# Kernel tuning notes

Hardware: AMD Instinct MI355X
Metric: run time of the kernel (lower is better)

Reference implementation:

```python
import jax, jax.numpy as jnp
import numpy as np

EPS = 1e-5
NEG = -1e9

def _ln(x, g, b):
    m = x.mean(-1, keepdims=True)
    v = ((x - m) ** 2).mean(-1, keepdims=True)
    return (x - m) / jnp.sqrt(v + EPS) * g + b

def setup_inputs() -> dict:
    key = jax.random.key(0)
    ks = jax.random.split(key, 32)
    B, N, D, F, L = 2, 512, 128, 512, 3
    s = 0.05
    rn = lambda k, sh, sc=s: jax.random.normal(k, sh, jnp.float32) * sc
    inp = {
        'rel_matrix': rn(ks[0], (B, N, N, 2), 1.0),
        'pre_w': rn(ks[1], (2, D)), 'pre_b': rn(ks[2], (D,)),
        'proj_w': rn(ks[3], (2 * D, D)), 'proj_b': rn(ks[4], (D,)),
        'out_w1': rn(ks[5], (D, D)),
        'bn_g': 1.0 + rn(ks[6], (D,)), 'bn_b': rn(ks[7], (D,)),
        'bn_m': rn(ks[8], (D,)),
        'bn_v': 0.5 + jax.random.uniform(ks[9], (D,), jnp.float32),
        'out_w2': rn(ks[10], (D, D)), 'out_b2': rn(ks[11], (D,)),
        'pe': rn(ks[12], (128, D)),
        'wq': rn(ks[13], (L, D, D)), 'bq': rn(ks[14], (L, D)),
        'wk': rn(ks[15], (L, D, D)), 'bk': rn(ks[16], (L, D)),
        'wv': rn(ks[17], (L, D, D)), 'bv': rn(ks[18], (L, D)),
        'wo': rn(ks[19], (L, D, D)), 'bo': rn(ks[20], (L, D)),
        'ln1g': jnp.ones((L, D), jnp.float32), 'ln1b': jnp.zeros((L, D), jnp.float32),
        'ln2g': jnp.ones((L, D), jnp.float32), 'ln2b': jnp.zeros((L, D), jnp.float32),
        'fw1': rn(ks[21], (L, D, F)), 'fb1': rn(ks[22], (L, F)),
        'fw2': rn(ks[23], (L, F, D)), 'fb2': rn(ks[24], (L, D)),
        'mask': jax.random.randint(ks[25], (B, N), 0, 2) > 0,
        'agent_id': jax.random.randint(ks[26], (B, N), 0, 128, dtype=jnp.int32),
    }
    return inp

def reference(rel_matrix, pre_w, pre_b, proj_w, proj_b, out_w1, bn_g, bn_b, bn_m, bn_v,
              out_w2, out_b2, pe, wq, bq, wk, bk, wv, bv, wo, bo,
              ln1g, ln1b, ln2g, ln2b, fw1, fb1, fw2, fb2, mask, agent_id):
    # --- pairwise relation chain (the headroom target) ---
    # symmetric pairwise validity mask (B,N,N)
    pm = (mask[:, None, :] & mask[:, :, None]).astype(rel_matrix.dtype)
    count = jnp.maximum(pm.sum(axis=2), 1.0)  # (B,N) valid-partner counts
    x = rel_matrix @ pre_w + pre_b            # (B,N,N,D) pre_proj Linear(2->128)
    pooled = jnp.einsum('bijd,bij->bid', x, pm) / count[..., None]  # masked mean over j
    x = jnp.concatenate([x, jnp.broadcast_to(pooled[:, :, None, :], x.shape)], axis=-1)
    x = x @ proj_w + proj_b                   # Linear(256->128)
    x = jnp.einsum('bijd,bij->bid', x, pm) / count[..., None]       # masked mean over j
    # out MLP: Linear(no bias) + BatchNorm1d(eval) + ReLU + Linear
    h = x @ out_w1
    h = (h - bn_m) / jnp.sqrt(bn_v + EPS) * bn_g + bn_b
    x = jax.nn.relu(h) @ out_w2 + out_b2
    x = x + pe[agent_id]                      # agent positional embedding
    # --- 3 post-norm single-head transformer layers (eval, dropout off) ---
    kbias = jnp.where(mask, 0.0, NEG)[:, None, :]  # key padding bias (B,1,N)
    scale = 1.0 / jnp.sqrt(jnp.asarray(x.shape[-1], x.dtype))
    for l in range(3):
        q = x @ wq[l] + bq[l]
        k = x @ wk[l] + bk[l]
        v = x @ wv[l] + bv[l]
        a = jax.nn.softmax(jnp.einsum('bid,bjd->bij', q, k) * scale + kbias, axis=-1)
        att = jnp.einsum('bij,bjd->bid', a, v) @ wo[l] + bo[l]
        x = _ln(x + att, ln1g[l], ln1b[l])
        ff = jax.nn.relu(x @ fw1[l] + fb1[l]) @ fw2[l] + fb2[l]
        x = _ln(x + ff, ln2g[l], ln2b[l])
    return x
```

## Files before the change

### kernel.cpp

```cpp
#include <hip/hip_runtime.h>
#include <hip/hip_bf16.h>

typedef unsigned short u16;
typedef unsigned int u32;
typedef unsigned char u8;
typedef __attribute__((ext_vector_type(8))) short bf16x8;
typedef __attribute__((ext_vector_type(4))) float f32x4;

#define DEV __device__ __forceinline__

DEV float bf2f(u16 u) { union { u32 i; float f; } c; c.i = ((u32)u) << 16; return c.f; }
DEV u16 f2bf(float f) {
  union { float f; u32 i; } c; c.f = f;
  u32 r = c.i + 0x7FFFu + ((c.i >> 16) & 1u);
  return (u16)(r >> 16);
}
DEV u32 pk2(float lo, float hi) { return (u32)f2bf(lo) | ((u32)f2bf(hi) << 16); }
DEV float rdsrc(const void* p, int e, int isb) {
  return isb ? bf2f(((const u16*)p)[e]) : ((const float*)p)[e];
}
DEV bf16x8 as_bf(uint4 v) { union { uint4 u; bf16x8 h; } c; c.u = v; return c.h; }

static constexpr int B = 2, N = 512, D = 128, F = 512;
static constexpr int NROW = B * N;
static constexpr float EPS = 1e-5f;
static constexpr float NEG = -1e9f;
static constexpr float SCALE = 0.08838834764831845f;

#define OFF_PRE_W   0
#define OFF_PRE_B   256
#define OFF_PROJ_B  33152
#define OFF_BN_G    49664
#define OFF_BN_B    49792
#define OFF_BN_M    49920
#define OFF_BN_V    50048
#define OFF_OUT_B2  66560
#define OFF_PE      66688
#define OFF_BQ      132224
#define OFF_BK      181760
#define OFF_BV      231296
#define OFF_BO      280832
#define OFF_LN1G    281216
#define OFF_LN1B    281600
#define OFF_LN2G    281984
#define OFF_LN2B    282368
#define OFF_FB1     479360
#define OFF_FB2     677504
#define W_TOTAL     677888

static constexpr int PB_PROJ = 0;
static constexpr int PB_OW1  = 8192;
static constexpr int PB_OW2  = 16384;
static constexpr int PB_L0   = 24576;
static constexpr int PB_LSTR = 98304;
static constexpr int PB_WO   = 24576;
static constexpr int PB_FW1  = 32768;
static constexpr int PB_FW2  = 65536;
static constexpr int PTOT    = 79872;

struct NEnt { const void* s; int off, n; };
struct PEnt { const void* s1; const void* s2; int o1, o2, dst, lgn, cum; };
struct PrepArgs { NEnt nrm[19]; PEnt pk[21]; };

template<int KT>
DEV f32x4 mmaK(const uint4* __restrict__ aPk, const uint4* __restrict__ Bp,
               int ncol, int col, int lane) {
  f32x4 acc = {0.f, 0.f, 0.f, 0.f};
  const int sub = lane >> 4;
  #pragma unroll
  for (int kt = 0; kt < KT; ++kt) {
    const int e8 = kt * 4 + sub;
    acc = __builtin_amdgcn_mfma_f32_16x16x32_bf16(
        as_bf(aPk[e8 * 16 + (lane & 15)]),
        as_bf(Bp[(size_t)e8 * ncol + col]),
        acc, 0, 0, 0);
  }
  return acc;
}

DEV void packA(const float* __restrict__ src, int ld, int K,
               uint4* __restrict__ aPk, int t) {
  const int n = (K >> 3) * 4;
  for (int i = t; i < n; i += 512) {
    const int e8 = i >> 2, r = i & 3;
    const float* s = src + r * ld + e8 * 8;
    uint4 w;
    w.x = pk2(s[0], s[1]); w.y = pk2(s[2], s[3]);
    w.z = pk2(s[4], s[5]); w.w = pk2(s[6], s[7]);
    aPk[e8 * 16 + r] = w;
  }
}

__global__ __launch_bounds__(256) void k_prep(PrepArgs pa,
    const void* __restrict__ bnv, const void* __restrict__ maskp,
    int* __restrict__ flags, int* __restrict__ mbuf,
    float* __restrict__ W, u32* __restrict__ Wb)
{
  const int t = threadIdx.x, bid = blockIdx.x;
  __shared__ int s_nb, s_m4, s_m2;
  if (t == 0) { s_nb = 0; s_m4 = 0; s_m2 = 0; }
  __syncthreads();
  if (t < 64) {
    const u32 w = ((const u32*)bnv)[t];
    if (((w >> 8) & 0xFFu) != 0x3Fu || ((w >> 24) & 0xFFu) != 0x3Fu)
      atomicOr(&s_nb, 1);
  }
  __syncthreads();
  const int isb = s_nb ? 0 : 1;

  if (bid < 16) {
    for (int ten = 0; ten < 19; ++ten) {
      const NEnt E = pa.nrm[ten];
      for (int e = bid * 256 + t; e < E.n; e += 16 * 256)
        W[E.off + e] = rdsrc(E.s, e, isb);
    }
  } else if (bid < 143) {
    for (int g = (bid - 16) * 256 + t; g < PTOT; g += 127 * 256) {
      int ei = 0;
      #pragma unroll
      for (int k = 1; k < 21; ++k) if (g >= pa.pk[k].cum) ei = k;
      const PEnt E = pa.pk[ei];
      const int li = g - E.cum;
      const int e8 = li >> E.lgn, c = li & ((1 << E.lgn) - 1);
      float f[8];
      #pragma unroll
      for (int i = 0; i < 8; ++i) {
        const int si = ((e8 * 8 + i) << E.lgn) + c;
        f[i] = rdsrc(E.s1, E.o1 + si, isb);
        if (E.s2) f[i] += rdsrc(E.s2, E.o2 + si, isb);
      }
      uint4 w;
      w.x = pk2(f[0], f[1]); w.y = pk2(f[2], f[3]);
      w.z = pk2(f[4], f[5]); w.w = pk2(f[6], f[7]);
      ((uint4*)(Wb + E.dst))[li] = w;
    }
  } else {
    {
      const u32 w = ((const u32*)maskp)[t];
      if (!(w == 0u || w == 1u || w == 0x3F800000u)) atomicOr(&s_m4, 1);
      if (!(w == 0u || w == 1u || w == 0x10000u || w == 0x10001u ||
            w == 0x3F80u || w == 0x3F800000u || w == 0x3F803F80u)) atomicOr(&s_m2, 1);
    }
    __syncthreads();
    const int mode = (!s_m4) ? 4 : ((!s_m2) ? 2 : 1);
    if (t == 0) { flags[0] = isb; flags[1] = mode; }
    #pragma unroll
    for (int k = 0; k < 4; ++k) {
      const int e = k * 256 + t;
      int v;
      if (mode == 4)      v = (((const u32*)maskp)[e] != 0u);
      else if (mode == 2) v = (((const u16*)maskp)[e] != 0);
      else                v = (((const u8*)maskp)[e]  != 0);
      mbuf[e] = v;
    }
  }
}

__global__ __launch_bounds__(512) void k_relq(
    const void* __restrict__ relv, const float* __restrict__ W,
    const u32* __restrict__ Wb,
    const int* __restrict__ flags, const int* __restrict__ mbuf,
    const int* __restrict__ agent_id, float* __restrict__ xbuf,
    float* __restrict__ qb, u32* __restrict__ kbT, u32* __restrict__ vbT)
{
  const int t = threadIdx.x;
  const int row0 = blockIdx.x * 4;
  const int b = row0 >> 9;
  const int wid = t >> 6;
  const int lane = t & 63;

  __shared__ float pl[4][D], zl[4][D], rl[4][D], os[4][D];
  __shared__ float pA[4][D], pB[4][D];
  __shared__ uint4 aPk[1024];
  __shared__ float wred[8][9];
  __shared__ float sT0[4], sT1[4], sMt;

  float s0[4] = {0, 0, 0, 0}, s1[4] = {0, 0, 0, 0}, cnt;
  {
    const int j = t;
    const float m = (float)mbuf[b * N + j];
    cnt = m;
    if (flags[0]) {
      const u32* rel2 = (const u32*)relv;
      #pragma unroll
      for (int r = 0; r < 4; ++r) {
        const u32 u = rel2[(size_t)(row0 + r) * N + j];
        s0[r] += m * bf2f((u16)(u & 0xFFFFu));
        s1[r] += m * bf2f((u16)(u >> 16));
      }
    } else {
      const float2* relf = (const float2*)relv;
      #pragma unroll
      for (int r = 0; r < 4; ++r) {
        const float2 u = relf[(size_t)(row0 + r) * N + j];
        s0[r] += m * u.x; s1[r] += m * u.y;
      }
    }
  }
  {
    const uint4 z = {0u, 0u, 0u, 0u};
    aPk[t] = z; aPk[t + 512] = z;
  }
  #pragma unroll
  for (int o = 32; o > 0; o >>= 1) {
    #pragma unroll
    for (int r = 0; r < 4; ++r) {
      s0[r] += __shfl_xor(s0[r], o, 64);
      s1[r] += __shfl_xor(s1[r], o, 64);
    }
    cnt += __shfl_xor(cnt, o, 64);
  }
  if ((t & 63) == 0) {
    #pragma unroll
    for (int r = 0; r < 4; ++r) { wred[wid][r] = s0[r]; wred[wid][4 + r] = s1[r]; }
    wred[wid][8] = cnt;
  }
  __syncthreads();
  if (t < 4) {
    float a0 = 0, a1 = 0;
    #pragma unroll
    for (int w = 0; w < 8; ++w) { a0 += wred[w][t]; a1 += wred[w][4 + t]; }
    sT0[t] = a0; sT1[t] = a1;
  }
  if (t == 8) {
    float c = 0;
    #pragma unroll
    for (int w = 0; w < 8; ++w) c += wred[w][8];
    sMt = c;
  }
  __syncthreads();

  {
    const int r = t >> 7, c = t & 127;
    const int mi = mbuf[row0 + r];
    pl[r][c] = mi ? (sT0[r] * W[OFF_PRE_W + c] + sT1[r] * W[OFF_PRE_W + D + c]) / sMt
                    + W[OFF_PRE_B + c]
                  : 0.f;
  }
  __syncthreads();

  packA(&pl[0][0], D, D, aPk, t);
  __syncthreads();
  {
    const int col = wid * 16 + (lane & 15);
    f32x4 acc = mmaK<4>(aPk, (const uint4*)(Wb + PB_PROJ), 128, col, lane);
    if (lane < 16) {
      #pragma unroll
      for (int g = 0; g < 4; ++g) pA[g][col] = acc[g];
    }
  }
  __syncthreads();
  {
    const int r = t >> 7, d = t & 127;
    zl[r][d] = mbuf[row0 + r] ? pA[r][d] + W[OFF_PROJ_B + d] : 0.f;
  }
  __syncthreads();

  packA(&zl[0][0], D, D, aPk, t);
  __syncthreads();
  {
    const int col = wid * 16 + (lane & 15);
    f32x4 acc = mmaK<4>(aPk, (const uint4*)(Wb + PB_OW1), 128, col, lane);
    if (lane < 16) {
      #pragma unroll
      for (int g = 0; g < 4; ++g) pA[g][col] = acc[g];
    }
  }
  __syncthreads();
  {
    const int r = t >> 7, d = t & 127;
    const float hb = (pA[r][d] - W[OFF_BN_M + d]) * __frsqrt_rn(W[OFF_BN_V + d] + EPS)
                     * W[OFF_BN_G + d] + W[OFF_BN_B + d];
    rl[r][d] = fmaxf(hb, 0.f);
  }
  __syncthreads();

  packA(&rl[0][0], D, D, aPk, t);
  __syncthreads();
  {
    const int col = wid * 16 + (lane & 15);
    f32x4 acc = mmaK<4>(aPk, (const uint4*)(Wb + PB_OW2), 128, col, lane);
    if (lane < 16) {
      #pragma unroll
      for (int g = 0; g < 4; ++g) pA[g][col] = acc[g];
    }
  }
  __syncthreads();
  {
    const int r = t >> 7, d = t & 127;
    const int aid = agent_id[row0 + r];
    const float x0 = pA[r][d] + W[OFF_OUT_B2 + d] + W[OFF_PE + aid * D + d];
    os[r][d] = x0;
    xbuf[(size_t)(row0 + r) * D + d] = x0;
  }
  __syncthreads();

  packA(&os[0][0], D, D, aPk, t);
  __syncthreads();
  {
    const int col = wid * 16 + (lane & 15);
    #pragma unroll
    for (int m = 0; m < 3; ++m) {
      f32x4 acc = mmaK<4>(aPk, (const uint4*)(Wb + PB_L0 + m * 8192), 128, col, lane);
      if (lane < 16) {
        const float bb = W[(m == 0 ? OFF_BQ : m == 1 ? OFF_BK : OFF_BV) + col];
        if (m == 0) {
          #pragma unroll
          for (int g = 0; g < 4; ++g) qb[(size_t)(row0 + g) * D + col] = acc[g] + bb;
        } else if (m == 1) {
          #pragma unroll
          for (int g = 0; g < 4; ++g) pA[g][col] = acc[g] + bb;
        } else {
          #pragma unroll
          for (int g = 0; g < 4; ++g) pB[g][col] = acc[g] + bb;
        }
      }
    }
  }
  __syncthreads();
  if (t < 64) {
    const int r = t >> 4, e8 = t & 15;
    const float* ks = pA[r];
    uint4 w;
    w.x = pk2(ks[8 * e8 + 0], ks[8 * e8 + 1]);
    w.y = pk2(ks[8 * e8 + 2], ks[8 * e8 + 3]);
    w.z = pk2(ks[8 * e8 + 4], ks[8 * e8 + 5]);
    w.w = pk2(ks[8 * e8 + 6], ks[8 * e8 + 7]);
    ((uint4*)kbT)[((size_t)b * 16 + e8) * 512 + (row0 & 511) + r] = w;
  }
  if (t < 128) {
    const int i0 = row0 & 511, j8 = i0 >> 3, h = (i0 >> 2) & 1;
    uint2 w;
    w.x = pk2(pB[0][t], pB[1][t]);
    w.y = pk2(pB[2][t], pB[3][t]);
    *(uint2*)(vbT + (((size_t)b * 64 + j8) * 128 + t) * 4 + 2 * h) = w;
  }
}

__global__ __launch_bounds__(512) void k_layer(
    const float* __restrict__ qin, const u32* __restrict__ kinT, const u32* __restrict__ vinT,
    const float* __restrict__ W, const u32* __restrict__ Wb, const int l, const int last,
    float* __restrict__ qout, u32* __restrict__ koutT, u32* __restrict__ voutT,
    const int* __restrict__ mbuf, float* __restrict__ xbuf, float* __restrict__ outp)
{
  const int t = threadIdx.x;
  const int row0 = blockIdx.x * 4;
  const int b = row0 >> 9;
  const int wid = t >> 6;
  const int lane = t & 63;

  const uint4* WOp = (const uint4*)(Wb + PB_L0 + l * PB_LSTR + PB_WO);
  const uint4* W1p = (const uint4*)(Wb + PB_L0 + l * PB_LSTR + PB_FW1);
  const uint4* W2p = (const uint4*)(Wb + PB_L0 + l * PB_LSTR + PB_FW2);
  const float* bo  = W + OFF_BO  + l * D;
  const float* g1  = W + OFF_LN1G + l * D;
  const float* b1  = W + OFF_LN1B + l * D;
  const float* fb1 = W + OFF_FB1 + l * F;
  const float* fb2 = W + OFF_FB2 + l * D;
  const float* g2  = W + OFF_LN2G + l * D;
  const float* b2v = W + OFF_LN2B + l * D;

  __shared__ float qs[4][D];
  __shared__ float p[4][N];
  __shared__ float hs[4][F];
  __shared__ float os[4][D];
  __shared__ float xs[4][D];
  __shared__ float pA[4][D], pB[4][D];
  __shared__ uint4 aPk[1024];
  __shared__ float den[4];

  {
    const int r = t >> 7, d = t & 127;
    qs[r][d] = qin[(size_t)(row0 + r) * D + d] * SCALE;
    const uint4 z = {0u, 0u, 0u, 0u};
    aPk[t] = z; aPk[t + 512] = z;
  }
  __syncthreads();

  packA(&qs[0][0], D, D, aPk, t);
  __syncthreads();
  {
    const uint4* Kp = (const uint4*)kinT + (size_t)b * 16 * 512;
    #pragma unroll
    for (int i = 0; i < 4; ++i) {
      const int col = (wid * 4 + i) * 16 + (lane & 15);
      f32x4 acc = mmaK<4>(aPk, Kp, 512, col, lane);
      if (lane < 16) {
        const float bias = mbuf[b * N + col] ? 0.f : NEG;
        #pragma unroll
        for (int g = 0; g < 4; ++g) p[g][col] = acc[g] + bias;
      }
    }
  }
  __syncthreads();

  if (wid < 4) {
    const int r = wid;
    float pv[8];
    float mx = -1e30f;
    #pragma unroll
    for (int k = 0; k < 8; ++k) { pv[k] = p[r][lane + 64 * k]; mx = fmaxf(mx, pv[k]); }
    #pragma unroll
    for (int o = 32; o > 0; o >>= 1) mx = fmaxf(mx, __shfl_xor(mx, o, 64));
    float sum = 0.f;
    #pragma unroll
    for (int k = 0; k < 8; ++k) { pv[k] = __expf(pv[k] - mx); sum += pv[k]; }
    #pragma unroll
    for (int o = 32; o > 0; o >>= 1) sum += __shfl_xor(sum, o, 64);
    #pragma unroll
    for (int k = 0; k < 8; ++k) p[r][lane + 64 * k] = pv[k];
    if (lane == 0) den[r] = sum;
  }
  __syncthreads();

  packA(&p[0][0], N, N, aPk, t);
  __syncthreads();
  {
    const int col = wid * 16 + (lane & 15);
    const uint4* Vp = (const uint4*)vinT + (size_t)b * 64 * 128;
    f32x4 acc = mmaK<16>(aPk, Vp, 128, col, lane);
    if (lane < 16) {
      #pragma unroll
      for (int g = 0; g < 4; ++g) os[g][col] = acc[g] / den[g];
    }
  }
  __syncthreads();

  packA(&os[0][0], D, D, aPk, t);
  __syncthreads();
  {
    const int col = wid * 16 + (lane & 15);
    f32x4 acc = mmaK<4>(aPk, WOp, 128, col, lane);
    if (lane < 16) {
      #pragma unroll
      for (int g = 0; g < 4; ++g) pA[g][col] = acc[g];
    }
  }
  __syncthreads();

  if (wid < 4) {
    const int r = wid;
    float tv[2];
    #pragma unroll
    for (int k = 0; k < 2; ++k) {
      const int d = lane + 64 * k;
      tv[k] = pA[r][d] + bo[d] + xbuf[(size_t)(row0 + r) * D + d];
    }
    float s = tv[0] + tv[1], sq = tv[0] * tv[0] + tv[1] * tv[1];
    #pragma unroll
    for (int o = 32; o > 0; o >>= 1) { s += __shfl_xor(s, o, 64); sq += __shfl_xor(sq, o, 64); }
    const float mean = s * (1.f / 128.f);
    const float var  = sq * (1.f / 128.f) - mean * mean;
    const float rstd = __frsqrt_rn(var + EPS);
    #pragma unroll
    for (int k = 0; k < 2; ++k) {
      const int d = lane + 64 * k;
      xs[r][d] = (tv[k] - mean) * rstd * g1[d] + b1[d];
    }
  }
  __syncthreads();

  packA(&xs[0][0], D, D, aPk, t);
  __syncthreads();
  {
    #pragma unroll
    for (int i = 0; i < 4; ++i) {
      const int col = (wid * 4 + i) * 16 + (lane & 15);
      f32x4 acc = mmaK<4>(aPk, W1p, 512, col, lane);
      if (lane < 16) {
        const float bb = fb1[col];
        #pragma unroll
        for (int g = 0; g < 4; ++g) hs[g][col] = fmaxf(acc[g] + bb, 0.f);
      }
    }
  }
  __syncthreads();

  packA(&hs[0][0], F, F, aPk, t);
  __syncthreads();
  {
    const int col = wid * 16 + (lane & 15);
    f32x4 acc = mmaK<16>(aPk, W2p, 128, col, lane);
    if (lane < 16) {
      #pragma unroll
      for (int g = 0; g < 4; ++g) pA[g][col] = acc[g];
    }
  }
  __syncthreads();

  if (wid < 4) {
    const int r = wid;
    float tv[2];
    #pragma unroll
    for (int k = 0; k < 2; ++k) {
      const int d = lane + 64 * k;
      tv[k] = pA[r][d] + fb2[d] + xs[r][d];
    }
    float s = tv[0] + tv[1], sq = tv[0] * tv[0] + tv[1] * tv[1];
    #pragma unroll
    for (int o = 32; o > 0; o >>= 1) { s += __shfl_xor(s, o, 64); sq += __shfl_xor(sq, o, 64); }
    const float mean = s * (1.f / 128.f);
    const float var  = sq * (1.f / 128.f) - mean * mean;
    const float rstd = __frsqrt_rn(var + EPS);
    #pragma unroll
    for (int k = 0; k < 2; ++k) {
      const int d = lane + 64 * k;
      const float xn = (tv[k] - mean) * rstd * g2[d] + b2v[d];
      os[r][d] = xn;
      xbuf[(size_t)(row0 + r) * D + d] = xn;
      if (outp) outp[(size_t)(row0 + r) * D + d] = xn;
    }
  }
  __syncthreads();

  if (!last) {
    packA(&os[0][0], D, D, aPk, t);
    __syncthreads();
    {
      const int col = wid * 16 + (lane & 15);
      #pragma unroll
      for (int m = 0; m < 3; ++m) {
        const uint4* Bp = (const uint4*)(Wb + PB_L0 + (l + 1) * PB_LSTR + m * 8192);
        f32x4 acc = mmaK<4>(aPk, Bp, 128, col, lane);
        if (lane < 16) {
          const float bb = W[(m == 0 ? OFF_BQ : m == 1 ? OFF_BK : OFF_BV) + (l + 1) * D + col];
          if (m == 0) {
            #pragma unroll
            for (int g = 0; g < 4; ++g) qout[(size_t)(row0 + g) * D + col] = acc[g] + bb;
          } else if (m == 1) {
            #pragma unroll
            for (int g = 0; g < 4; ++g) pA[g][col] = acc[g] + bb;
          } else {
            #pragma unroll
            for (int g = 0; g < 4; ++g) pB[g][col] = acc[g] + bb;
          }
        }
      }
    }
    __syncthreads();
    if (t < 64) {
      const int r = t >> 4, e8 = t & 15;
      const float* ks = pA[r];
      uint4 w;
      w.x = pk2(ks[8 * e8 + 0], ks[8 * e8 + 1]);
      w.y = pk2(ks[8 * e8 + 2], ks[8 * e8 + 3]);
      w.z = pk2(ks[8 * e8 + 4], ks[8 * e8 + 5]);
      w.w = pk2(ks[8 * e8 + 6], ks[8 * e8 + 7]);
      ((uint4*)koutT)[((size_t)b * 16 + e8) * 512 + (row0 & 511) + r] = w;
    }
    if (t < 128) {
      const int i0 = row0 & 511, j8 = i0 >> 3, h = (i0 >> 2) & 1;
      uint2 w;
      w.x = pk2(pB[0][t], pB[1][t]);
      w.y = pk2(pB[2][t], pB[3][t]);
      *(uint2*)(voutT + (((size_t)b * 64 + j8) * 128 + t) * 4 + 2 * h) = w;
    }
  }
}

extern "C" void kernel_launch(void* const* d_in, const int* in_sizes, int n_in,
                              void* d_out, int out_size, void* d_ws, size_t ws_size,
                              hipStream_t stream) {
  int*   flags = (int*)d_ws;
  int*   mbuf  = flags + 16;
  float* xbuf  = (float*)d_ws + 1040;
  float* q0    = xbuf + NROW * D;
  float* q1    = q0 + NROW * D;
  u32*   kT0   = (u32*)(q1 + NROW * D);
  u32*   kT1   = kT0 + 65536;
  u32*   vT0   = kT1 + 65536;
  u32*   vT1   = vT0 + 65536;
  float* W     = (float*)(vT1 + 65536);
  u32*   Wb    = (u32*)(W + W_TOTAL);

  PrepArgs pa;
  {
    const NEnt nrm[19] = {
      {d_in[1],  OFF_PRE_W,  256}, {d_in[2],  OFF_PRE_B, 128},
      {d_in[4],  OFF_PROJ_B, 128},
      {d_in[6],  OFF_BN_G,   128}, {d_in[7],  OFF_BN_B,  128},
      {d_in[8],  OFF_BN_M,   128}, {d_in[9],  OFF_BN_V,  128},
      {d_in[11], OFF_OUT_B2, 128}, {d_in[12], OFF_PE,  16384},
      {d_in[14], OFF_BQ,     384}, {d_in[16], OFF_BK,    384},
      {d_in[18], OFF_BV,     384}, {d_in[20], OFF_BO,    384},
      {d_in[21], OFF_LN1G,   384}, {d_in[22], OFF_LN1B,  384},
      {d_in[23], OFF_LN2G,   384}, {d_in[24], OFF_LN2B,  384},
      {d_in[26], OFF_FB1,   1536}, {d_in[28], OFF_FB2,   384}};
    for (int i = 0; i < 19; ++i) pa.nrm[i] = nrm[i];

    pa.pk[0] = {d_in[3], d_in[3], 0, 16384, PB_PROJ, 7, 0};
    pa.pk[1] = {d_in[5],  nullptr, 0, 0, PB_OW1, 7, 2048};
    pa.pk[2] = {d_in[10], nullptr, 0, 0, PB_OW2, 7, 4096};
    for (int l = 0; l < 3; ++l) {
      const int lb = PB_L0 + l * PB_LSTR;
      const int cl = 6144 + l * 24576;
      pa.pk[3 + 6 * l + 0] = {d_in[13], nullptr, l * 16384, 0, lb,          7, cl};
      pa.pk[3 + 6 * l + 1] = {d_in[15], nullptr, l * 16384, 0, lb + 8192,   7, cl + 2048};
      pa.pk[3 + 6 * l + 2] = {d_in[17], nullptr, l * 16384, 0, lb + 16384,  7, cl + 4096};
      pa.pk[3 + 6 * l + 3] = {d_in[19], nullptr, l * 16384, 0, lb + PB_WO,  7, cl + 6144};
      pa.pk[3 + 6 * l + 4] = {d_in[25], nullptr, l * 65536, 0, lb + PB_FW1, 9, cl + 8192};
      pa.pk[3 + 6 * l + 5] = {d_in[27], nullptr, l * 65536, 0, lb + PB_FW2, 7, cl + 16384};
    }
  }
  const int* agent_id = (const int*)d_in[30];

  k_prep<<<144, 256, 0, stream>>>(pa, d_in[9], d_in[29], flags, mbuf, W, Wb);
  k_relq<<<NROW / 4, 512, 0, stream>>>(d_in[0], W, Wb, flags, mbuf, agent_id, xbuf,
                                       q0, kT0, vT0);

  float* qs_[2] = {q0, q1};
  u32*   ks_[2] = {kT0, kT1};
  u32*   vs_[2] = {vT0, vT1};
  for (int l = 0; l < 3; ++l) {
    const int cur = l & 1, nxt = cur ^ 1;
    const int last = (l == 2);
    k_layer<<<NROW / 4, 512, 0, stream>>>(
        qs_[cur], ks_[cur], vs_[cur],
        W, Wb, l, last,
        qs_[nxt], ks_[nxt], vs_[nxt],
        mbuf, xbuf, last ? (float*)d_out : (float*)nullptr);
  }
}
```

Before: 77.32 us.

## Double layer kernel threads with split-K MMA and widen weight-pack grid

The transformer layer kernel now runs with 1024 threads per block instead of 512. The long-K matmuls (P·V, W_O and FFN2) are split across two halves of the waves, with partial sums written to pA/pB and added afterwards, and the N-wide matmuls now give each wave two column tiles instead of four. Separately, the prep kernel's weight-packing grid grows from 127 to 495 blocks. The aim is to shorten each block's serial MFMA chain and add latency hiding, at the cost of extra reduction passes, a larger block and possible occupancy limits.

```diff
diff --git a/kernel.cpp b/kernel.cpp
--- a/kernel.cpp
+++ b/kernel.cpp
@@ -63,13 +63,13 @@
 struct PrepArgs { NEnt nrm[19]; PEnt pk[21]; };
 
 template<int KT>
-DEV f32x4 mmaK(const uint4* __restrict__ aPk, const uint4* __restrict__ Bp,
-               int ncol, int col, int lane) {
+DEV f32x4 mmaKo(const uint4* __restrict__ aPk, const uint4* __restrict__ Bp,
+                int ncol, int col, int lane, int kt0) {
   f32x4 acc = {0.f, 0.f, 0.f, 0.f};
   const int sub = lane >> 4;
   #pragma unroll
   for (int kt = 0; kt < KT; ++kt) {
-    const int e8 = kt * 4 + sub;
+    const int e8 = (kt0 + kt) * 4 + sub;
     acc = __builtin_amdgcn_mfma_f32_16x16x32_bf16(
         as_bf(aPk[e8 * 16 + (lane & 15)]),
         as_bf(Bp[(size_t)e8 * ncol + col]),
@@ -79,9 +79,9 @@
 }
 
 DEV void packA(const float* __restrict__ src, int ld, int K,
-               uint4* __restrict__ aPk, int t) {
+               uint4* __restrict__ aPk, int t, int nthr) {
   const int n = (K >> 3) * 4;
-  for (int i = t; i < n; i += 512) {
+  for (int i = t; i < n; i += nthr) {
     const int e8 = i >> 2, r = i & 3;
     const float* s = src + r * ld + e8 * 8;
     uint4 w;
@@ -114,8 +114,8 @@
       for (int e = bid * 256 + t; e < E.n; e += 16 * 256)
         W[E.off + e] = rdsrc(E.s, e, isb);
     }
-  } else if (bid < 143) {
-    for (int g = (bid - 16) * 256 + t; g < PTOT; g += 127 * 256) {
+  } else if (bid < 511) {
+    for (int g = (bid - 16) * 256 + t; g < PTOT; g += 495 * 256) {
       int ei = 0;
       #pragma unroll
       for (int k = 1; k < 21; ++k) if (g >= pa.pk[k].cum) ei = k;
@@ -239,11 +239,11 @@
   }
   __syncthreads();
 
-  packA(&pl[0][0], D, D, aPk, t);
+  packA(&pl[0][0], D, D, aPk, t, 512);
   __syncthreads();
   {
     const int col = wid * 16 + (lane & 15);
-    f32x4 acc = mmaK<4>(aPk, (const uint4*)(Wb + PB_PROJ), 128, col, lane);
+    f32x4 acc = mmaKo<4>(aPk, (const uint4*)(Wb + PB_PROJ), 128, col, lane, 0);
     if (lane < 16) {
       #pragma unroll
       for (int g = 0; g < 4; ++g) pA[g][col] = acc[g];
@@ -256,11 +256,11 @@
   }
   __syncthreads();
 
-  packA(&zl[0][0], D, D, aPk, t);
+  packA(&zl[0][0], D, D, aPk, t, 512);
   __syncthreads();
   {
     const int col = wid * 16 + (lane & 15);
-    f32x4 acc = mmaK<4>(aPk, (const uint4*)(Wb + PB_OW1), 128, col, lane);
+    f32x4 acc = mmaKo<4>(aPk, (const uint4*)(Wb + PB_OW1), 128, col, lane, 0);
     if (lane < 16) {
       #pragma unroll
       for (int g = 0; g < 4; ++g) pA[g][col] = acc[g];
@@ -275,11 +275,11 @@
   }
   __syncthreads();
 
-  packA(&rl[0][0], D, D, aPk, t);
+  packA(&rl[0][0], D, D, aPk, t, 512);
   __syncthreads();
   {
     const int col = wid * 16 + (lane & 15);
-    f32x4 acc = mmaK<4>(aPk, (const uint4*)(Wb + PB_OW2), 128, col, lane);
+    f32x4 acc = mmaKo<4>(aPk, (const uint4*)(Wb + PB_OW2), 128, col, lane, 0);
     if (lane < 16) {
       #pragma unroll
       for (int g = 0; g < 4; ++g) pA[g][col] = acc[g];
@@ -295,13 +295,13 @@
   }
   __syncthreads();
 
-  packA(&os[0][0], D, D, aPk, t);
+  packA(&os[0][0], D, D, aPk, t, 512);
   __syncthreads();
   {
     const int col = wid * 16 + (lane & 15);
     #pragma unroll
     for (int m = 0; m < 3; ++m) {
-      f32x4 acc = mmaK<4>(aPk, (const uint4*)(Wb + PB_L0 + m * 8192), 128, col, lane);
+      f32x4 acc = mmaKo<4>(aPk, (const uint4*)(Wb + PB_L0 + m * 8192), 128, col, lane, 0);
       if (lane < 16) {
         const float bb = W[(m == 0 ? OFF_BQ : m == 1 ? OFF_BK : OFF_BV) + col];
         if (m == 0) {
@@ -337,7 +337,7 @@
   }
 }
 
-__global__ __launch_bounds__(512) void k_layer(
+__global__ __launch_bounds__(1024) void k_layer(
     const float* __restrict__ qin, const u32* __restrict__ kinT, const u32* __restrict__ vinT,
     const float* __restrict__ W, const u32* __restrict__ Wb, const int l, const int last,
     float* __restrict__ qout, u32* __restrict__ koutT, u32* __restrict__ voutT,
@@ -348,6 +348,7 @@
   const int b = row0 >> 9;
   const int wid = t >> 6;
   const int lane = t & 63;
+  const int w8 = wid & 7, half = wid >> 3;
 
   const uint4* WOp = (const uint4*)(Wb + PB_L0 + l * PB_LSTR + PB_WO);
   const uint4* W1p = (const uint4*)(Wb + PB_L0 + l * PB_LSTR + PB_FW1);
@@ -361,34 +362,35 @@
   const float* b2v = W + OFF_LN2B + l * D;
 
   __shared__ float qs[4][D];
-  __shared__ float p[4][N];
-  __shared__ float hs[4][F];
+  __shared__ float bufA[4][512];
   __shared__ float os[4][D];
   __shared__ float xs[4][D];
   __shared__ float pA[4][D], pB[4][D];
   __shared__ uint4 aPk[1024];
   __shared__ float den[4];
 
-  {
+  if (t < 512) {
     const int r = t >> 7, d = t & 127;
     qs[r][d] = qin[(size_t)(row0 + r) * D + d] * SCALE;
+  }
+  {
     const uint4 z = {0u, 0u, 0u, 0u};
-    aPk[t] = z; aPk[t + 512] = z;
-  }
-  __syncthreads();
-
-  packA(&qs[0][0], D, D, aPk, t);
+    aPk[t & 1023] = z;
+  }
+  __syncthreads();
+
+  packA(&qs[0][0], D, D, aPk, t, 1024);
   __syncthreads();
   {
     const uint4* Kp = (const uint4*)kinT + (size_t)b * 16 * 512;
     #pragma unroll
-    for (int i = 0; i < 4; ++i) {
-      const int col = (wid * 4 + i) * 16 + (lane & 15);
-      f32x4 acc = mmaK<4>(aPk, Kp, 512, col, lane);
+    for (int ii = 0; ii < 2; ++ii) {
+      const int col = (wid + 16 * ii) * 16 + (lane & 15);
+      f32x4 acc = mmaKo<4>(aPk, Kp, 512, col, lane, 0);
       if (lane < 16) {
         const float bias = mbuf[b * N + col] ? 0.f : NEG;
         #pragma unroll
-        for (int g = 0; g < 4; ++g) p[g][col] = acc[g] + bias;
+        for (int g = 0; g < 4; ++g) bufA[g][col] = acc[g] + bias;
       }
     }
   }
@@ -399,7 +401,7 @@
     float pv[8];
     float mx = -1e30f;
     #pragma unroll
-    for (int k = 0; k < 8; ++k) { pv[k] = p[r][lane + 64 * k]; mx = fmaxf(mx, pv[k]); }
+    for (int k = 0; k < 8; ++k) { pv[k] = bufA[r][lane + 64 * k]; mx = fmaxf(mx, pv[k]); }
     #pragma unroll
     for (int o = 32; o > 0; o >>= 1) mx = fmaxf(mx, __shfl_xor(mx, o, 64));
     float sum = 0.f;
@@ -408,32 +410,39 @@
     #pragma unroll
     for (int o = 32; o > 0; o >>= 1) sum += __shfl_xor(sum, o, 64);
     #pragma unroll
-    for (int k = 0; k < 8; ++k) p[r][lane + 64 * k] = pv[k];
+    for (int k = 0; k < 8; ++k) bufA[r][lane + 64 * k] = pv[k];
     if (lane == 0) den[r] = sum;
   }
   __syncthreads();
 
-  packA(&p[0][0], N, N, aPk, t);
-  __syncthreads();
-  {
-    const int col = wid * 16 + (lane & 15);
+  packA(&bufA[0][0], N, N, aPk, t, 1024);
+  __syncthreads();
+  {
+    const int col = w8 * 16 + (lane & 15);
     const uint4* Vp = (const uint4*)vinT + (size_t)b * 64 * 128;
-    f32x4 acc = mmaK<16>(aPk, Vp, 128, col, lane);
+    f32x4 acc = mmaKo<8>(aPk, Vp, 128, col, lane, half * 8);
     if (lane < 16) {
-      #pragma unroll
-      for (int g = 0; g < 4; ++g) os[g][col] = acc[g] / den[g];
-    }
-  }
-  __syncthreads();
-
-  packA(&os[0][0], D, D, aPk, t);
-  __syncthreads();
-  {
-    const int col = wid * 16 + (lane & 15);
-    f32x4 acc = mmaK<4>(aPk, WOp, 128, col, lane);
+      float* dst = half ? &pB[0][0] : &pA[0][0];
+      #pragma unroll
+      for (int g = 0; g < 4; ++g) dst[g * D + col] = acc[g];
+    }
+  }
+  __syncthreads();
+  if (t < 512) {
+    const int r = t >> 7, d = t & 127;
+    os[r][d] = (pA[r][d] + pB[r][d]) / den[r];
+  }
+  __syncthreads();
+
+  packA(&os[0][0], D, D, aPk, t, 1024);
+  __syncthreads();
+  {
+    const int col = w8 * 16 + (lane & 15);
+    f32x4 acc = mmaKo<2>(aPk, WOp, 128, col, lane, half * 2);
     if (lane < 16) {
-      #pragma unroll
-      for (int g = 0; g < 4; ++g) pA[g][col] = acc[g];
+      float* dst = half ? &pB[0][0] : &pA[0][0];
+      #pragma unroll
+      for (int g = 0; g < 4; ++g) dst[g * D + col] = acc[g];
     }
   }
   __syncthreads();
@@ -444,7 +453,7 @@
     #pragma unroll
     for (int k = 0; k < 2; ++k) {
       const int d = lane + 64 * k;
-      tv[k] = pA[r][d] + bo[d] + xbuf[(size_t)(row0 + r) * D + d];
+      tv[k] = pA[r][d] + pB[r][d] + bo[d] + xbuf[(size_t)(row0 + r) * D + d];
     }
     float s = tv[0] + tv[1], sq = tv[0] * tv[0] + tv[1] * tv[1];
     #pragma unroll
@@ -460,30 +469,31 @@
   }
   __syncthreads();
 
-  packA(&xs[0][0], D, D, aPk, t);
-  __syncthreads();
-  {
-    #pragma unroll
-    for (int i = 0; i < 4; ++i) {
-      const int col = (wid * 4 + i) * 16 + (lane & 15);
-      f32x4 acc = mmaK<4>(aPk, W1p, 512, col, lane);
+  packA(&xs[0][0], D, D, aPk, t, 1024);
+  __syncthreads();
+  {
+    #pragma unroll
+    for (int ii = 0; ii < 2; ++ii) {
+      const int col = (wid + 16 * ii) * 16 + (lane & 15);
+      f32x4 acc = mmaKo<4>(aPk, W1p, 512, col, lane, 0);
       if (lane < 16) {
         const float bb = fb1[col];
         #pragma unroll
-        for (int g = 0; g < 4; ++g) hs[g][col] = fmaxf(acc[g] + bb, 0.f);
+        for (int g = 0; g < 4; ++g) bufA[g][col] = fmaxf(acc[g] + bb, 0.f);
       }
     }
   }
   __syncthreads();
 
-  packA(&hs[0][0], F, F, aPk, t);
-  __syncthreads();
-  {
-    const int col = wid * 16 + (lane & 15);
-    f32x4 acc = mmaK<16>(aPk, W2p, 128, col, lane);
+  packA(&bufA[0][0], F, F, aPk, t, 1024);
+  __syncthreads();
+  {
+    const int col = w8 * 16 + (lane & 15);
+    f32x4 acc = mmaKo<8>(aPk, W2p, 128, col, lane, half * 8);
     if (lane < 16) {
-      #pragma unroll
-      for (int g = 0; g < 4; ++g) pA[g][col] = acc[g];
+      float* dst = half ? &pB[0][0] : &pA[0][0];
+      #pragma unroll
+      for (int g = 0; g < 4; ++g) dst[g * D + col] = acc[g];
     }
   }
   __syncthreads();
@@ -494,7 +504,7 @@
     #pragma unroll
     for (int k = 0; k < 2; ++k) {
       const int d = lane + 64 * k;
-      tv[k] = pA[r][d] + fb2[d] + xs[r][d];
+      tv[k] = pA[r][d] + pB[r][d] + fb2[d] + xs[r][d];
     }
     float s = tv[0] + tv[1], sq = tv[0] * tv[0] + tv[1] * tv[1];
     #pragma unroll
@@ -508,20 +518,22 @@
       const float xn = (tv[k] - mean) * rstd * g2[d] + b2v[d];
       os[r][d] = xn;
       xbuf[(size_t)(row0 + r) * D + d] = xn;
-      if (outp) outp[(size_t)(row0 + r) * D + d] = xn;
+      if (last) outp[(size_t)(row0 + r) * D + d] = xn;
     }
   }
   __syncthreads();
 
   if (!last) {
-    packA(&os[0][0], D, D, aPk, t);
+    packA(&os[0][0], D, D, aPk, t, 1024);
     __syncthreads();
-    {
-      const int col = wid * 16 + (lane & 15);
-      #pragma unroll
-      for (int m = 0; m < 3; ++m) {
+    #pragma unroll
+    for (int it = 0; it < 2; ++it) {
+      const int task = wid + 16 * it;
+      if (task < 24) {
+        const int m = task >> 3, c8 = task & 7;
+        const int col = c8 * 16 + (lane & 15);
         const uint4* Bp = (const uint4*)(Wb + PB_L0 + (l + 1) * PB_LSTR + m * 8192);
-        f32x4 acc = mmaK<4>(aPk, Bp, 128, col, lane);
+        f32x4 acc = mmaKo<4>(aPk, Bp, 128, col, lane, 0);
         if (lane < 16) {
           const float bb = W[(m == 0 ? OFF_BQ : m == 1 ? OFF_BK : OFF_BV) + (l + 1) * D + col];
           if (m == 0) {
@@ -604,7 +616,7 @@
   }
   const int* agent_id = (const int*)d_in[30];
 
-  k_prep<<<144, 256, 0, stream>>>(pa, d_in[9], d_in[29], flags, mbuf, W, Wb);
+  k_prep<<<512, 256, 0, stream>>>(pa, d_in[9], d_in[29], flags, mbuf, W, Wb);
   k_relq<<<NROW / 4, 512, 0, stream>>>(d_in[0], W, Wb, flags, mbuf, agent_id, xbuf,
                                        q0, kT0, vT0);
 
@@ -614,7 +626,7 @@
   for (int l = 0; l < 3; ++l) {
     const int cur = l & 1, nxt = cur ^ 1;
     const int last = (l == 2);
-    k_layer<<<NROW / 4, 512, 0, stream>>>(
+    k_layer<<<NROW / 4, 1024, 0, stream>>>(
         qs_[cur], ks_[cur], vs_[cur],
         W, Wb, l, last,
         qs_[nxt], ks_[nxt], vs_[nxt],
```

Measured after the change: 67.80 us. -12.3%, faster.
